# Performance work log

Measured on AMD Instinct MI355X. Metric: run time of the kernel, lower is better.

## Reference

```python
import jax, jax.numpy as jnp
import numpy as np

N, DEG, F, H, O, B = 100000, 16, 128, 128, 128, 8192


def setup_inputs() -> dict:
    key = jax.random.key(0)
    k1, k2, k3, k4, k5 = jax.random.split(key, 5)
    features = jax.random.normal(k1, (N, F), dtype=jnp.float32)
    w1 = jax.random.normal(k2, (2 * F, H), dtype=jnp.float32)
    w2 = jax.random.normal(k3, (2 * H, O), dtype=jnp.float32)
    neighbor_idx = jax.random.randint(k4, (N, DEG), 0, N, dtype=jnp.int32)
    nodes = jax.random.randint(k5, (B,), 0, N, dtype=jnp.int32)
    return {"features": features, "w1": w1, "w2": w2,
            "neighbor_idx": neighbor_idx, "nodes": nodes}


def reference(features, w1, w2, neighbor_idx, nodes):
    # Layer 1 (computed for all nodes, vectorized): mean-aggregate neighbor
    # raw features, concat with self features, project with w1.
    neigh_feat = features[neighbor_idx]                 # [N, DEG, F] gather
    agg1 = neigh_feat.mean(axis=1)                      # [N, F]
    h1 = jnp.concatenate([features, agg1], axis=-1) @ w1  # [N, H]

    # Layer 2 (batch nodes): mean-aggregate neighbor layer-1 embeddings,
    # concat with self layer-1 embedding, project with w2.
    h1_self = h1[nodes]                                 # [B, H]
    h1_neigh = h1[neighbor_idx[nodes]].mean(axis=1)     # [B, H]
    out = jnp.concatenate([h1_self, h1_neigh], axis=-1) @ w2  # [B, O]
    return out
```

## Files before the change

### kernel.cpp

```cpp
#include <hip/hip_runtime.h>


#define N_NODES 100000
#define DEG     16
#define FDIM    128
#define HDIM    128
#define B_NODES 8192

typedef __attribute__((ext_vector_type(8))) short bf16x8;
typedef __attribute__((ext_vector_type(8))) unsigned short u16x8;
typedef __attribute__((ext_vector_type(4))) float f32x4;
typedef __attribute__((ext_vector_type(2))) float f32x2;

static __device__ __forceinline__ unsigned short f2bf(float f) {
    union { float f; unsigned u; } v; v.f = f;
    unsigned r = v.u + 0x7fff + ((v.u >> 16) & 1);
    return (unsigned short)(r >> 16);
}
static __device__ __forceinline__ float bf2f(unsigned short b) {
    union { unsigned u; float f; } v; v.u = ((unsigned)b) << 16;
    return v.f;
}

__global__ __launch_bounds__(256)
void prep(const float* __restrict__ feat, const float* __restrict__ w1,
          const float* __restrict__ w2, unsigned short* __restrict__ fb,
          unsigned char* __restrict__ f8,
          unsigned short* __restrict__ w1T, unsigned short* __restrict__ w2T) {
    if (blockIdx.x < 6250) {
        long e = ((long)blockIdx.x * 256 + threadIdx.x) * 8;
        float4 v0 = *(const float4*)(feat + e);
        float4 v1 = *(const float4*)(feat + e + 4);
        u16x8 ob;
        ob[0] = f2bf(v0.x); ob[1] = f2bf(v0.y); ob[2] = f2bf(v0.z); ob[3] = f2bf(v0.w);
        ob[4] = f2bf(v1.x); ob[5] = f2bf(v1.y); ob[6] = f2bf(v1.z); ob[7] = f2bf(v1.w);
        *(u16x8*)(fb + e) = ob;
        int p0 = 0, p1 = 0;
        p0 = __builtin_amdgcn_cvt_pk_fp8_f32(v0.x, v0.y, p0, false);
        p0 = __builtin_amdgcn_cvt_pk_fp8_f32(v0.z, v0.w, p0, true);
        p1 = __builtin_amdgcn_cvt_pk_fp8_f32(v1.x, v1.y, p1, false);
        p1 = __builtin_amdgcn_cvt_pk_fp8_f32(v1.z, v1.w, p1, true);
        uint2 o8; o8.x = (unsigned)p0; o8.y = (unsigned)p1;
        *(uint2*)(f8 + e) = o8;
    } else {
        int bid = blockIdx.x - 6250;
        const float* w = (bid < 8) ? w1 : w2;
        unsigned short* wT = (bid < 8) ? w1T : w2T;
        int kb = (bid & 7) * 32;
        int n = threadIdx.x & 127, dk = threadIdx.x >> 7;
#pragma unroll
        for (int i = 0; i < 16; ++i) {
            int k = kb + dk * 16 + i;
            wT[n * 256 + k] = f2bf(w[k * 128 + n]);
        }
    }
}

__global__ __launch_bounds__(256)
void k1_agg(const unsigned char* __restrict__ f8, const int* __restrict__ nbr,
            unsigned short* __restrict__ agg) {
    const int t = threadIdx.x;
    const int node = blockIdx.x * 16 + (t >> 4);
    const int cg = (t & 15) * 8;
    const int* idx = nbr + node * DEG;
    float s[8] = {0.f, 0.f, 0.f, 0.f, 0.f, 0.f, 0.f, 0.f};
#pragma unroll
    for (int d = 0; d < DEG; ++d) {
        int nb = idx[d];
        uint2 v = *(const uint2*)(f8 + (long)nb * FDIM + cg);
        f32x2 a0 = __builtin_amdgcn_cvt_pk_f32_fp8((int)v.x, false);
        f32x2 a1 = __builtin_amdgcn_cvt_pk_f32_fp8((int)v.x, true);
        f32x2 a2 = __builtin_amdgcn_cvt_pk_f32_fp8((int)v.y, false);
        f32x2 a3 = __builtin_amdgcn_cvt_pk_f32_fp8((int)v.y, true);
        s[0] += a0[0]; s[1] += a0[1]; s[2] += a1[0]; s[3] += a1[1];
        s[4] += a2[0]; s[5] += a2[1]; s[6] += a3[0]; s[7] += a3[1];
    }
    u16x8 o;
#pragma unroll
    for (int j = 0; j < 8; ++j) o[j] = f2bf(s[j] * 0.0625f);
    *(u16x8*)(agg + node * 128 + cg) = o;
}

__global__ __launch_bounds__(256, 3)
void g1(const unsigned short* __restrict__ fb, const unsigned short* __restrict__ agg,
        const unsigned short* __restrict__ w1T, unsigned short* __restrict__ h1) {
    const int t = threadIdx.x, wave = t >> 6, lane = t & 63;
    const int m16 = lane & 15, quad = lane >> 4;
    const int row0 = blockIdx.x * 128;
    const int n0 = wave * 32;

    bf16x8 B[8][2];
#pragma unroll
    for (int kc = 0; kc < 8; ++kc)
#pragma unroll
        for (int nt = 0; nt < 2; ++nt)
            B[kc][nt] = *(const bf16x8*)(w1T + (n0 + nt * 16 + m16) * 256 + kc * 32 + quad * 8);

    for (int c = 0; c < 4; ++c) {
        const int r0 = row0 + c * 32;
        bf16x8 A[2][8];
#pragma unroll
        for (int mt = 0; mt < 2; ++mt) {
            int grow = r0 + mt * 16 + m16;
            bool ok = grow < N_NODES;
            const unsigned short* pf = fb + (long)grow * 128 + quad * 8;
            const unsigned short* pa = agg + (long)grow * 128 + quad * 8;
            bf16x8 z = {};
#pragma unroll
            for (int kc = 0; kc < 4; ++kc)
                A[mt][kc] = ok ? *(const bf16x8*)(pf + kc * 32) : z;
#pragma unroll
            for (int kc = 4; kc < 8; ++kc)
                A[mt][kc] = ok ? *(const bf16x8*)(pa + (kc - 4) * 32) : z;
        }

        f32x4 acc[2][2] = {};
#pragma unroll
        for (int kc = 0; kc < 8; ++kc)
#pragma unroll
            for (int mt = 0; mt < 2; ++mt)
#pragma unroll
                for (int nt = 0; nt < 2; ++nt)
                    acc[mt][nt] = __builtin_amdgcn_mfma_f32_16x16x32_bf16(A[mt][kc], B[kc][nt], acc[mt][nt], 0, 0, 0);

#pragma unroll
        for (int mt = 0; mt < 2; ++mt)
#pragma unroll
            for (int reg = 0; reg < 4; ++reg) {
                int grow = r0 + mt * 16 + quad * 4 + reg;
                if (grow >= N_NODES) continue;
#pragma unroll
                for (int nt = 0; nt < 2; ++nt)
                    h1[grow * HDIM + n0 + nt * 16 + m16] = f2bf(acc[mt][nt][reg]);
            }
    }
}

__global__ __launch_bounds__(256)
void g2_fused(const unsigned short* __restrict__ h1, const unsigned short* __restrict__ w2T,
              const int* __restrict__ nbr, const int* __restrict__ nodes,
              float* __restrict__ out) {
    __shared__ unsigned short X2[64][264];
    const int t = threadIdx.x, wave = t >> 6, lane = t & 63;
    const int m16 = lane & 15, quad = lane >> 4;
    const int b0 = blockIdx.x * 64;
    const int colb = m16 * 8;

    for (int g = 0; g < 4; ++g) {
        int Ln = wave * 16 + g * 4 + quad;
        int node = nodes[b0 + Ln];
        *(u16x8*)(&X2[Ln][colb]) = *(const u16x8*)(h1 + node * HDIM + colb);
        const int* idx = nbr + node * DEG;
        float s[8] = {0.f, 0.f, 0.f, 0.f, 0.f, 0.f, 0.f, 0.f};
#pragma unroll
        for (int d = 0; d < DEG; ++d) {
            int nb = idx[d];
            u16x8 v = *(const u16x8*)(h1 + nb * HDIM + colb);
#pragma unroll
            for (int j = 0; j < 8; ++j) s[j] += bf2f(v[j]);
        }
        u16x8 o;
#pragma unroll
        for (int j = 0; j < 8; ++j) o[j] = f2bf(s[j] * 0.0625f);
        *(u16x8*)(&X2[Ln][128 + colb]) = o;
    }
    __syncthreads();

    f32x4 acc[8] = {};
#pragma unroll
    for (int kc = 0; kc < 8; ++kc) {
        bf16x8 a = *(const bf16x8*)(&X2[wave * 16 + m16][kc * 32 + quad * 8]);
#pragma unroll
        for (int nt = 0; nt < 8; ++nt) {
            bf16x8 b = *(const bf16x8*)(w2T + (nt * 16 + m16) * 256 + kc * 32 + quad * 8);
            acc[nt] = __builtin_amdgcn_mfma_f32_16x16x32_bf16(a, b, acc[nt], 0, 0, 0);
        }
    }

#pragma unroll
    for (int nt = 0; nt < 8; ++nt)
#pragma unroll
        for (int reg = 0; reg < 4; ++reg) {
            int row = b0 + wave * 16 + quad * 4 + reg;
            out[row * 128 + nt * 16 + m16] = acc[nt][reg];
        }
}

extern "C" void kernel_launch(void* const* d_in, const int* in_sizes, int n_in,
                              void* d_out, int out_size, void* d_ws, size_t ws_size,
                              hipStream_t stream) {
    const float* feat  = (const float*)d_in[0];
    const float* w1    = (const float*)d_in[1];
    const float* w2    = (const float*)d_in[2];
    const int*   nbr   = (const int*)d_in[3];
    const int*   nodes = (const int*)d_in[4];
    float* out = (float*)d_out;

    char* ws = (char*)d_ws;
    unsigned short* fb  = (unsigned short*)ws;
    unsigned char*  f8  = (unsigned char*)(ws + 25600000);
    unsigned short* agg = (unsigned short*)(ws + 38400000);
    unsigned short* h1  = (unsigned short*)(ws + 64000000);
    unsigned short* w1T = (unsigned short*)(ws + 89600000);
    unsigned short* w2T = (unsigned short*)(ws + 89665536);

    prep<<<6266, 256, 0, stream>>>(feat, w1, w2, fb, f8, w1T, w2T);
    k1_agg<<<6250, 256, 0, stream>>>(f8, nbr, agg);
    g1<<<(N_NODES + 127) / 128, 256, 0, stream>>>(fb, agg, w1T, h1);
    g2_fused<<<B_NODES / 64, 256, 0, stream>>>(h1, w2T, nbr, nodes, out);
}
```

Baseline: 185.6 us.

## Stage w1 in LDS and double-buffer A-chunk loads in g1

The g1 GEMM kernel now copies the whole transposed w1 into shared memory once per block and reads B fragments from LDS instead of holding them in registers. It also double-buffers the per-chunk A fragment loads, prefetching the next 32-row chunk's features and aggregates while the current chunk's MFMAs run. The aim is to hide global-load latency on the A operand. In exchange it uses about 66 KB of LDS per block, lowers the occupancy hint from 3 to 2 blocks, and doubles the A register footprint.

```diff
diff --git a/kernel.cpp b/kernel.cpp
--- a/kernel.cpp
+++ b/kernel.cpp
@@ -81,24 +81,27 @@
     *(u16x8*)(agg + node * 128 + cg) = o;
 }
 
-__global__ __launch_bounds__(256, 3)
+__global__ __launch_bounds__(256, 2)
 void g1(const unsigned short* __restrict__ fb, const unsigned short* __restrict__ agg,
         const unsigned short* __restrict__ w1T, unsigned short* __restrict__ h1) {
+    __shared__ unsigned short W[128][264];
     const int t = threadIdx.x, wave = t >> 6, lane = t & 63;
     const int m16 = lane & 15, quad = lane >> 4;
     const int row0 = blockIdx.x * 128;
     const int n0 = wave * 32;
 
-    bf16x8 B[8][2];
-#pragma unroll
-    for (int kc = 0; kc < 8; ++kc)
-#pragma unroll
-        for (int nt = 0; nt < 2; ++nt)
-            B[kc][nt] = *(const bf16x8*)(w1T + (n0 + nt * 16 + m16) * 256 + kc * 32 + quad * 8);
-
-    for (int c = 0; c < 4; ++c) {
+#pragma unroll
+    for (int i = 0; i < 16; ++i) {
+        int e = i * 2048 + t * 8;
+        int n = e >> 8, k = e & 255;
+        *(u16x8*)(&W[n][k]) = *(const u16x8*)(w1T + e);
+    }
+    __syncthreads();
+
+    bf16x8 A[2][2][8];
+
+    auto load_chunk = [&](int c, bf16x8 (*Ad)[8]) {
         const int r0 = row0 + c * 32;
-        bf16x8 A[2][8];
 #pragma unroll
         for (int mt = 0; mt < 2; ++mt) {
             int grow = r0 + mt * 16 + m16;
@@ -107,22 +110,29 @@
             const unsigned short* pa = agg + (long)grow * 128 + quad * 8;
             bf16x8 z = {};
 #pragma unroll
-            for (int kc = 0; kc < 4; ++kc)
-                A[mt][kc] = ok ? *(const bf16x8*)(pf + kc * 32) : z;
-#pragma unroll
-            for (int kc = 4; kc < 8; ++kc)
-                A[mt][kc] = ok ? *(const bf16x8*)(pa + (kc - 4) * 32) : z;
-        }
-
+            for (int kc = 0; kc < 4; ++kc) Ad[mt][kc] = ok ? *(const bf16x8*)(pf + kc * 32) : z;
+#pragma unroll
+            for (int kc = 0; kc < 4; ++kc) Ad[mt][4 + kc] = ok ? *(const bf16x8*)(pa + kc * 32) : z;
+        }
+    };
+
+    load_chunk(0, A[0]);
+
+#pragma unroll
+    for (int c = 0; c < 4; ++c) {
+        if (c < 3) load_chunk(c + 1, A[(c + 1) & 1]);
+        bf16x8 (*Ac)[8] = A[c & 1];
         f32x4 acc[2][2] = {};
 #pragma unroll
-        for (int kc = 0; kc < 8; ++kc)
-#pragma unroll
-            for (int mt = 0; mt < 2; ++mt)
-#pragma unroll
-                for (int nt = 0; nt < 2; ++nt)
-                    acc[mt][nt] = __builtin_amdgcn_mfma_f32_16x16x32_bf16(A[mt][kc], B[kc][nt], acc[mt][nt], 0, 0, 0);
-
+        for (int kc = 0; kc < 8; ++kc) {
+            bf16x8 b0 = *(const bf16x8*)(&W[n0 + m16][kc * 32 + quad * 8]);
+            bf16x8 b1 = *(const bf16x8*)(&W[n0 + 16 + m16][kc * 32 + quad * 8]);
+            acc[0][0] = __builtin_amdgcn_mfma_f32_16x16x32_bf16(Ac[0][kc], b0, acc[0][0], 0, 0, 0);
+            acc[1][0] = __builtin_amdgcn_mfma_f32_16x16x32_bf16(Ac[1][kc], b0, acc[1][0], 0, 0, 0);
+            acc[0][1] = __builtin_amdgcn_mfma_f32_16x16x32_bf16(Ac[0][kc], b1, acc[0][1], 0, 0, 0);
+            acc[1][1] = __builtin_amdgcn_mfma_f32_16x16x32_bf16(Ac[1][kc], b1, acc[1][1], 0, 0, 0);
+        }
+        const int r0 = row0 + c * 32;
 #pragma unroll
         for (int mt = 0; mt < 2; ++mt)
 #pragma unroll
```

Result: no change. 182.5 us (-1.7%).
